# Performance work log

Hardware: AMD Instinct MI355X
Metric: run time of the kernel (lower is better)

Reference implementation:

```python
import jax, jax.numpy as jnp
import numpy as np

B, D, O = 512, 256, 128  # batch, input_dim, output_dim


def setup_inputs() -> dict:
    key = jax.random.key(0)
    k1, k2, k3, k4, k5, k6 = jax.random.split(key, 6)
    eyeD = jnp.eye(D, dtype=jnp.float32)
    # density-like inputs: diagonal offset keeps the trace denominator well-conditioned
    x_real = jax.random.normal(k1, (B, D, D), dtype=jnp.float32) + 2.0 * eyeD
    x_imag = jax.random.normal(k2, (B, D, D), dtype=jnp.float32)
    # weight = identity + small perturbation (module inits to [eye, zeros] stacked)
    w_r = eyeD + 0.02 * jax.random.normal(k3, (D, D), dtype=jnp.float32)
    w_i = 0.02 * jax.random.normal(k4, (D, D), dtype=jnp.float32)
    weight = jnp.stack([w_r, w_i], axis=-1)  # [D, D, 2]
    rand_w = jax.random.uniform(k5, (O,), dtype=jnp.float32)
    lam = jax.random.uniform(k6, (1,), dtype=jnp.float32)
    return {"x_real": x_real, "x_imag": x_imag, "weight": weight,
            "rand_w": rand_w, "lam": lam}


def reference(x_real, x_imag, weight, rand_w, lam):
    out_dim = rand_w.shape[0]
    U_r = weight[:, :, 0]  # [D, D]
    U_i = weight[:, :, 1]
    # evolution: (U_r + i U_i) X (U_r + i U_i)^H, batched over b
    R = jnp.einsum('ij,bjk->bik', U_r, x_real) - jnp.einsum('ij,bjk->bik', U_i, x_imag)
    I = jnp.einsum('ij,bjk->bik', U_i, x_real) + jnp.einsum('ij,bjk->bik', U_r, x_imag)
    out_r = jnp.einsum('bik,jk->bij', R, U_r) + jnp.einsum('bik,jk->bij', I, U_i)
    out_i = jnp.einsum('bik,jk->bij', I, U_r) - jnp.einsum('bik,jk->bij', R, U_i)
    # input_dim >= output_dim branch: top-left block, normalized by trace of real part
    sub_r = out_r[:, :out_dim, :out_dim]
    sub_i = out_i[:, :out_dim, :out_dim]
    tr = jnp.trace(sub_r, axis1=1, axis2=2)[:, None, None]  # [B,1,1]
    norm_r = sub_r / tr
    norm_i = sub_i / tr
    p = jax.nn.softmax(rand_w, axis=-1)
    s = jax.nn.sigmoid(lam[0])
    output_r = s * norm_r + (1.0 - s) * jnp.diag(p)
    output_i = s * norm_i
    return (output_r, output_i)
```

## Files before the change

### kernel.cpp

```cpp
#include <hip/hip_runtime.h>
#include <hip/hip_bf16.h>


typedef __attribute__((ext_vector_type(4))) float f32x4;
typedef __attribute__((ext_vector_type(8))) short bf16x8;

static __device__ __forceinline__ short f2bf(float f) {
    unsigned u = __float_as_uint(f);
    u += 0x7fffu + ((u >> 16) & 1u);
    return (short)(u >> 16);
}

static __device__ __forceinline__ unsigned cvtpk2(float lo, float hi) {
    union { __hip_bfloat162 h; unsigned u; } c;
    c.h = __float22bfloat162_rn(float2{lo, hi});
    return c.u;
}

static __device__ __forceinline__ bf16x8 pack8(f32x4 a, f32x4 b) {
    union { unsigned u[4]; bf16x8 v; } r;
    r.u[0] = cvtpk2(a[0], a[1]);
    r.u[1] = cvtpk2(a[2], a[3]);
    r.u[2] = cvtpk2(b[0], b[1]);
    r.u[3] = cvtpk2(b[2], b[3]);
    return r.v;
}

static __device__ __forceinline__ f32x4 mfma16(bf16x8 a, bf16x8 b, f32x4 c) {
    return __builtin_amdgcn_mfma_f32_16x16x32_bf16(a, b, c, 0, 0, 0);
}

#define XGOFF(S) (((S) >> 3) * 16384 + ((S) & 7) * 32)

__global__ void qprep_u(const float* __restrict__ wt,
                        short* __restrict__ Ur, short* __restrict__ Ui) {
    int idx = blockIdx.x * 256 + threadIdx.x;
    float2 v = ((const float2*)wt)[idx];
    Ur[idx] = f2bf(v.x);
    Ui[idx] = f2bf(v.y);
}

__global__ void qprep_ps(const float* __restrict__ rw, const float* __restrict__ lm,
                         float* __restrict__ pv, float* __restrict__ sv) {
    int t = threadIdx.x;
    float w0 = rw[t], w1 = rw[t + 64];
    float m = fmaxf(w0, w1);
    #pragma unroll
    for (int o = 32; o > 0; o >>= 1) m = fmaxf(m, __shfl_xor(m, o));
    float e0 = expf(w0 - m), e1 = expf(w1 - m);
    float ss = e0 + e1;
    #pragma unroll
    for (int o = 32; o > 0; o >>= 1) ss += __shfl_xor(ss, o);
    pv[t] = e0 / ss;
    pv[t + 64] = e1 / ss;
    if (t == 0) sv[0] = 1.f / (1.f + expf(-lm[0]));
}

__global__ void qprep_q(const float* __restrict__ wt,
                        short* __restrict__ Qrb, short* __restrict__ Qib) {
    int j = blockIdx.x;
    int k = threadIdx.x;
    float ar = 0.f, ai = 0.f;
    for (int i = 0; i < 128; ++i) {
        float2 uk = ((const float2*)wt)[i * 256 + k];
        float2 uj = ((const float2*)wt)[i * 256 + j];
        ar += uk.x * uj.x + uk.y * uj.y;
        ai += uk.x * uj.y - uk.y * uj.x;
    }
    Qrb[j * 256 + k] = f2bf(ar);
    Qib[j * 256 + k] = f2bf(ai);
}

template<int P>
static __device__ __forceinline__ void phaseT(
    char* smem, const float* xgR, const float* xgI, int stW,
    int rdo0, int rdo1, const short* qbr, const short* qbi,
    int kb, int c16, int g4, bool dotr,
    f32x4* genR, f32x4* genI, bf16x8* qgr, bf16x8* qgi,
    f32x4* yR, f32x4* yI, f32x4& tr4)
{
    if (P + 1 < 32) {
        char* sb = smem + 65536 + ((P + 1) & 1) * 16384;
        *(f32x4*)(sb + stW)        = genR[(P + 1) & 3];
        *(f32x4*)(sb + 8192 + stW) = genI[(P + 1) & 3];
    }
    if (dotr && (P + 1 < 32)) {
        qgr[(P + 1) & 1] = *(const bf16x8*)(qbr + XGOFF(P + 1));
        qgi[(P + 1) & 1] = *(const bf16x8*)(qbi + XGOFF(P + 1));
    }
    if (P + 5 < 32) {
        genR[(P + 5) & 3] = *(const f32x4*)(xgR + XGOFF(P + 5));
        genI[(P + 5) & 3] = *(const f32x4*)(xgI + XGOFF(P + 5));
    }
    asm volatile("" ::: "memory");
    {
        char* rb = smem + 65536 + (P & 1) * 16384;
        f32x4 a0 = *(const f32x4*)(rb + rdo0);
        f32x4 a1 = *(const f32x4*)(rb + rdo1);
        f32x4 b0 = *(const f32x4*)(rb + 8192 + rdo0);
        f32x4 b1 = *(const f32x4*)(rb + 8192 + rdo1);
        bf16x8 axr  = pack8(a0, a1);
        bf16x8 axi  = pack8(b0, b1);
        bf16x8 axrn = axr ^ (short)0x8000;
        {
            const int kloc = kb + c16;
            const int uo = kloc * 512 + (((P & 7) * 64 + g4 * 16) ^ ((kloc & 7) << 4));
            bf16x8 bur = *(const bf16x8*)(smem + uo);
            bf16x8 bui = *(const bf16x8*)(smem + 32768 + uo);
            yR[0] = mfma16(axr,  bur, yR[0]);
            yR[0] = mfma16(axi,  bui, yR[0]);
            yI[0] = mfma16(axi,  bur, yI[0]);
            yI[0] = mfma16(axrn, bui, yI[0]);
        }
        {
            const int kloc = kb + 16 + c16;
            const int uo = kloc * 512 + (((P & 7) * 64 + g4 * 16) ^ ((kloc & 7) << 4));
            bf16x8 bur = *(const bf16x8*)(smem + uo);
            bf16x8 bui = *(const bf16x8*)(smem + 32768 + uo);
            yR[1] = mfma16(axr,  bur, yR[1]);
            yR[1] = mfma16(axi,  bui, yR[1]);
            yI[1] = mfma16(axi,  bur, yI[1]);
            yI[1] = mfma16(axrn, bui, yI[1]);
        }
        if (dotr) {
            bf16x8 axin = axi ^ (short)0x8000;
            tr4 = mfma16(axr,  qgr[P & 1], tr4);
            tr4 = mfma16(axin, qgi[P & 1], tr4);
        }
    }
    asm volatile("s_waitcnt lgkmcnt(0)" ::: "memory");
    __builtin_amdgcn_sched_barrier(0);
    __builtin_amdgcn_s_barrier();
    __builtin_amdgcn_sched_barrier(0);
}

static __device__ __forceinline__ void stageB(
    char* smem, const short* Urg, const short* Uig, int jt,
    int wm, int wn, int c16, int g4,
    f32x4 (&sR)[2][2], f32x4 (&sI)[2][2])
{
    #pragma unroll
    for (int ks2 = 0; ks2 < 2; ++ks2) {
        bf16x8 aur[2], aui[2], auin[2];
        #pragma unroll
        for (int mt = 0; mt < 2; ++mt) {
            int i = wm * 32 + mt * 16 + c16;
            aur[mt]  = *(const bf16x8*)(Urg + (size_t)i * 256 + jt + ks2 * 32 + g4 * 8);
            aui[mt]  = *(const bf16x8*)(Uig + (size_t)i * 256 + jt + ks2 * 32 + g4 * 8);
            auin[mt] = aui[mt] ^ (short)0x8000;
        }
        #pragma unroll
        for (int nt2 = 0; nt2 < 2; ++nt2) {
            int kloc = wn * 32 + nt2 * 16 + c16;
            int off  = kloc * 128 + ((ks2 * 64 + g4 * 16) ^ ((kloc & 7) << 4));
            bf16x8 byr = *(const bf16x8*)(smem + 98304 + off);
            bf16x8 byi = *(const bf16x8*)(smem + 106496 + off);
            #pragma unroll
            for (int mt = 0; mt < 2; ++mt) {
                sR[mt][nt2] = mfma16(aur[mt],  byr, sR[mt][nt2]);
                sR[mt][nt2] = mfma16(auin[mt], byi, sR[mt][nt2]);
                sI[mt][nt2] = mfma16(aui[mt],  byr, sI[mt][nt2]);
                sI[mt][nt2] = mfma16(aur[mt],  byi, sI[mt][nt2]);
            }
        }
    }
}

#define YT_AND_B(JT) do {                                                       \
    {                                                                           \
        const int klA = kb + c16;                                               \
        const int oA  = klA * 128 + ((ja * 2 + g4 * 8) ^ ((klA & 7) << 4));     \
        uint2 v;                                                                \
        v.x = cvtpk2(yR[0][0], yR[0][1]); v.y = cvtpk2(yR[0][2], yR[0][3]);     \
        *(uint2*)(smem + 98304 + oA) = v;                                       \
        v.x = cvtpk2(yI[0][0], yI[0][1]); v.y = cvtpk2(yI[0][2], yI[0][3]);     \
        *(uint2*)(smem + 106496 + oA) = v;                                      \
        const int klB = kb + 16 + c16;                                          \
        const int oB  = klB * 128 + ((ja * 2 + g4 * 8) ^ ((klB & 7) << 4));     \
        v.x = cvtpk2(yR[1][0], yR[1][1]); v.y = cvtpk2(yR[1][2], yR[1][3]);     \
        *(uint2*)(smem + 98304 + oB) = v;                                       \
        v.x = cvtpk2(yI[1][0], yI[1][1]); v.y = cvtpk2(yI[1][2], yI[1][3]);     \
        *(uint2*)(smem + 106496 + oB) = v;                                      \
    }                                                                           \
    asm volatile("s_waitcnt lgkmcnt(0)" ::: "memory");                          \
    __builtin_amdgcn_sched_barrier(0);                                          \
    __builtin_amdgcn_s_barrier();                                               \
    __builtin_amdgcn_sched_barrier(0);                                          \
    stageB(smem, Urg, Uig, (JT) * 64, wm, wn, c16, g4, sR, sI);                 \
    yR[0] = zero; yR[1] = zero; yI[0] = zero; yI[1] = zero;                     \
} while (0)

#define PH(P) phaseT<P>(smem, xgR, xgI, stW, rdo0, rdo1, qbr, qbi, kb, c16, g4, \
                        dotr, genR, genI, qgr, qgi, yR, yI, tr4)

__global__ __launch_bounds__(512, 2) void qfused(
    const float* __restrict__ xr, const float* __restrict__ xi,
    const short* __restrict__ Urg, const short* __restrict__ Uig,
    const short* __restrict__ Qrb, const short* __restrict__ Qib,
    const float* __restrict__ pv, const float* __restrict__ sv,
    float* __restrict__ out)
{
    __shared__ __align__(16) char smem[114688];

    const int bx   = blockIdx.x;
    const int b    = bx >> 1;
    const int kh   = bx & 1;
    const int tid  = threadIdx.x;
    const int lane = tid & 63;
    const int w    = tid >> 6;
    const int c16  = lane & 15;
    const int g4   = lane >> 4;

    #pragma unroll
    for (int q = 0; q < 4; ++q) {
        int c    = tid + q * 512;
        int row  = c >> 5;
        int slot = c & 31;
        int ss   = slot ^ (row & 7);
        const short* sr = Urg + (size_t)(kh * 64 + row) * 256 + ss * 8;
        const short* si = Uig + (size_t)(kh * 64 + row) * 256 + ss * 8;
        *(bf16x8*)(smem + row * 512 + slot * 16)         = *(const bf16x8*)sr;
        *(bf16x8*)(smem + 32768 + row * 512 + slot * 16) = *(const bf16x8*)si;
    }

    const float* xrb = xr + ((size_t)b << 16);
    const float* xib = xi + ((size_t)b << 16);

    const int  ja   = (w & 3) * 16;
    const int  kb   = (w >> 2) * 32;
    const int  wm   = w >> 1;
    const int  wn   = w & 1;
    const bool dotr = (w < 4);

    const int rowW = w * 8 + (lane >> 3);
    const int cW   = lane & 7;
    const float* xgR = xrb + rowW * 256 + cW * 4;
    const float* xgI = xib + rowW * 256 + cW * 4;
    const int stW  = rowW * 128 + ((cW ^ (rowW & 7)) << 4);

    const int rA   = ja + c16;
    const int rdo0 = rA * 128 + (((2 * g4)     ^ (rA & 7)) << 4);
    const int rdo1 = rA * 128 + (((2 * g4 + 1) ^ (rA & 7)) << 4);

    const short* qbr = Qrb + (size_t)(ja + c16) * 256 + g4 * 8;
    const short* qbi = Qib + (size_t)(ja + c16) * 256 + g4 * 8;

    f32x4 zero = {0.f, 0.f, 0.f, 0.f};
    f32x4 sR[2][2], sI[2][2];
    #pragma unroll
    for (int m = 0; m < 2; ++m)
        #pragma unroll
        for (int n = 0; n < 2; ++n) { sR[m][n] = zero; sI[m][n] = zero; }
    f32x4 tr4 = zero;
    f32x4 yR[2], yI[2];
    yR[0] = zero; yR[1] = zero; yI[0] = zero; yI[1] = zero;

    f32x4 genR[4], genI[4];
    bf16x8 qgr[2], qgi[2];

    {
        f32x4 t0R = *(const f32x4*)(xgR + XGOFF(0));
        f32x4 t0I = *(const f32x4*)(xgI + XGOFF(0));
        genR[1] = *(const f32x4*)(xgR + XGOFF(1));
        genI[1] = *(const f32x4*)(xgI + XGOFF(1));
        genR[2] = *(const f32x4*)(xgR + XGOFF(2));
        genI[2] = *(const f32x4*)(xgI + XGOFF(2));
        genR[3] = *(const f32x4*)(xgR + XGOFF(3));
        genI[3] = *(const f32x4*)(xgI + XGOFF(3));
        genR[0] = *(const f32x4*)(xgR + XGOFF(4));
        genI[0] = *(const f32x4*)(xgI + XGOFF(4));
        if (dotr) {
            qgr[0] = *(const bf16x8*)(qbr + XGOFF(0));
            qgi[0] = *(const bf16x8*)(qbi + XGOFF(0));
        }
        *(f32x4*)(smem + 65536 + stW)        = t0R;
        *(f32x4*)(smem + 65536 + 8192 + stW) = t0I;
    }
    __syncthreads();

    PH(0);  PH(1);  PH(2);  PH(3);  PH(4);  PH(5);  PH(6);  PH(7);
    YT_AND_B(0);
    PH(8);  PH(9);  PH(10); PH(11); PH(12); PH(13); PH(14); PH(15);
    YT_AND_B(1);
    PH(16); PH(17); PH(18); PH(19); PH(20); PH(21); PH(22); PH(23);
    YT_AND_B(2);
    PH(24); PH(25); PH(26); PH(27); PH(28); PH(29); PH(30); PH(31);
    YT_AND_B(3);

    float loc = (dotr && ((c16 >> 2) == g4)) ? tr4[c16 & 3] : 0.f;
    #pragma unroll
    for (int o = 32; o > 0; o >>= 1) loc += __shfl_xor(loc, o);
    __syncthreads();
    float* red = (float*)(smem + 65536);
    if (lane == 0) red[w] = loc;
    __syncthreads();
    float tr = red[0] + red[1] + red[2] + red[3] + red[4] + red[5] + red[6] + red[7];

    float s     = sv[0];
    float inv   = s / tr;
    float onems = 1.f - s;
    float* outr = out + (size_t)b * 16384;
    float* outi = out + 8388608 + (size_t)b * 16384;

    #pragma unroll
    for (int mt = 0; mt < 2; ++mt)
        #pragma unroll
        for (int nt2 = 0; nt2 < 2; ++nt2) {
            int colc = kh * 64 + wn * 32 + nt2 * 16 + c16;
            #pragma unroll
            for (int r = 0; r < 4; ++r) {
                int row = wm * 32 + mt * 16 + g4 * 4 + r;
                float vr = sR[mt][nt2][r] * inv;
                if (row == colc) vr += onems * pv[row];
                outr[row * 128 + colc] = vr;
                outi[row * 128 + colc] = sI[mt][nt2][r] * inv;
            }
        }
}

extern "C" void kernel_launch(void* const* d_in, const int* in_sizes, int n_in,
                              void* d_out, int out_size, void* d_ws, size_t ws_size,
                              hipStream_t stream) {
    (void)in_sizes; (void)n_in; (void)out_size; (void)ws_size;
    const float* xr = (const float*)d_in[0];
    const float* xi = (const float*)d_in[1];
    const float* wt = (const float*)d_in[2];
    const float* rw = (const float*)d_in[3];
    const float* lm = (const float*)d_in[4];

    short* Ur  = (short*)d_ws;
    short* Ui  = Ur + 32768;
    float* pv  = (float*)((char*)d_ws + 131072);
    float* sv  = pv + 128;
    short* Qrb = (short*)((char*)d_ws + 135168);
    short* Qib = (short*)((char*)d_ws + 266240);
    float* o   = (float*)d_out;

    qprep_u<<<dim3(128), dim3(256), 0, stream>>>(wt, Ur, Ui);
    qprep_ps<<<dim3(1), dim3(64), 0, stream>>>(rw, lm, pv, sv);
    qprep_q<<<dim3(256), dim3(256), 0, stream>>>(wt, Qrb, Qib);
    qfused<<<dim3(1024), dim3(512), 0, stream>>>(xr, xi, Ur, Ui, Qrb, Qib, pv, sv, o);
}
```

Baseline: 175.4 us.

## Load X fragments directly from global into MFMA layout, drop LDS staging

```diff
diff --git a/kernel.cpp b/kernel.cpp
--- a/kernel.cpp
+++ b/kernel.cpp
@@ -73,69 +73,57 @@
 
 template<int P>
 static __device__ __forceinline__ void phaseT(
-    char* smem, const float* xgR, const float* xgI, int stW,
-    int rdo0, int rdo1, const short* qbr, const short* qbi,
+    const char* smem, const float* xgR, const float* xgI,
+    const short* qbr, const short* qbi,
     int kb, int c16, int g4, bool dotr,
-    f32x4* genR, f32x4* genI, bf16x8* qgr, bf16x8* qgi,
+    f32x4* gRa, f32x4* gRb, f32x4* gIa, f32x4* gIb,
+    bf16x8* qgr, bf16x8* qgi,
     f32x4* yR, f32x4* yI, f32x4& tr4)
 {
-    if (P + 1 < 32) {
-        char* sb = smem + 65536 + ((P + 1) & 1) * 16384;
-        *(f32x4*)(sb + stW)        = genR[(P + 1) & 3];
-        *(f32x4*)(sb + 8192 + stW) = genI[(P + 1) & 3];
+    if (P + 2 < 32) {
+        constexpr int S = (P + 2 < 32) ? P + 2 : 0;
+        gRa[S % 3] = *(const f32x4*)(xgR + XGOFF(S));
+        gRb[S % 3] = *(const f32x4*)(xgR + XGOFF(S) + 4);
+        gIa[S % 3] = *(const f32x4*)(xgI + XGOFF(S));
+        gIb[S % 3] = *(const f32x4*)(xgI + XGOFF(S) + 4);
     }
     if (dotr && (P + 1 < 32)) {
         qgr[(P + 1) & 1] = *(const bf16x8*)(qbr + XGOFF(P + 1));
         qgi[(P + 1) & 1] = *(const bf16x8*)(qbi + XGOFF(P + 1));
     }
-    if (P + 5 < 32) {
-        genR[(P + 5) & 3] = *(const f32x4*)(xgR + XGOFF(P + 5));
-        genI[(P + 5) & 3] = *(const f32x4*)(xgI + XGOFF(P + 5));
-    }
     asm volatile("" ::: "memory");
+    bf16x8 axr  = pack8(gRa[P % 3], gRb[P % 3]);
+    bf16x8 axi  = pack8(gIa[P % 3], gIb[P % 3]);
+    bf16x8 axrn = axr ^ (short)0x8000;
     {
-        char* rb = smem + 65536 + (P & 1) * 16384;
-        f32x4 a0 = *(const f32x4*)(rb + rdo0);
-        f32x4 a1 = *(const f32x4*)(rb + rdo1);
-        f32x4 b0 = *(const f32x4*)(rb + 8192 + rdo0);
-        f32x4 b1 = *(const f32x4*)(rb + 8192 + rdo1);
-        bf16x8 axr  = pack8(a0, a1);
-        bf16x8 axi  = pack8(b0, b1);
-        bf16x8 axrn = axr ^ (short)0x8000;
-        {
-            const int kloc = kb + c16;
-            const int uo = kloc * 512 + (((P & 7) * 64 + g4 * 16) ^ ((kloc & 7) << 4));
-            bf16x8 bur = *(const bf16x8*)(smem + uo);
-            bf16x8 bui = *(const bf16x8*)(smem + 32768 + uo);
-            yR[0] = mfma16(axr,  bur, yR[0]);
-            yR[0] = mfma16(axi,  bui, yR[0]);
-            yI[0] = mfma16(axi,  bur, yI[0]);
-            yI[0] = mfma16(axrn, bui, yI[0]);
-        }
-        {
-            const int kloc = kb + 16 + c16;
-            const int uo = kloc * 512 + (((P & 7) * 64 + g4 * 16) ^ ((kloc & 7) << 4));
-            bf16x8 bur = *(const bf16x8*)(smem + uo);
-            bf16x8 bui = *(const bf16x8*)(smem + 32768 + uo);
-            yR[1] = mfma16(axr,  bur, yR[1]);
-            yR[1] = mfma16(axi,  bui, yR[1]);
-            yI[1] = mfma16(axi,  bur, yI[1]);
-            yI[1] = mfma16(axrn, bui, yI[1]);
-        }
-        if (dotr) {
-            bf16x8 axin = axi ^ (short)0x8000;
-            tr4 = mfma16(axr,  qgr[P & 1], tr4);
-            tr4 = mfma16(axin, qgi[P & 1], tr4);
-        }
-    }
-    asm volatile("s_waitcnt lgkmcnt(0)" ::: "memory");
-    __builtin_amdgcn_sched_barrier(0);
-    __builtin_amdgcn_s_barrier();
-    __builtin_amdgcn_sched_barrier(0);
+        const int kloc = kb + c16;
+        const int uo = kloc * 512 + (((P & 7) * 64 + g4 * 16) ^ ((kloc & 7) << 4));
+        bf16x8 bur = *(const bf16x8*)(smem + uo);
+        bf16x8 bui = *(const bf16x8*)(smem + 32768 + uo);
+        yR[0] = mfma16(axr,  bur, yR[0]);
+        yR[0] = mfma16(axi,  bui, yR[0]);
+        yI[0] = mfma16(axi,  bur, yI[0]);
+        yI[0] = mfma16(axrn, bui, yI[0]);
+    }
+    {
+        const int kloc = kb + 16 + c16;
+        const int uo = kloc * 512 + (((P & 7) * 64 + g4 * 16) ^ ((kloc & 7) << 4));
+        bf16x8 bur = *(const bf16x8*)(smem + uo);
+        bf16x8 bui = *(const bf16x8*)(smem + 32768 + uo);
+        yR[1] = mfma16(axr,  bur, yR[1]);
+        yR[1] = mfma16(axi,  bui, yR[1]);
+        yI[1] = mfma16(axi,  bur, yI[1]);
+        yI[1] = mfma16(axrn, bui, yI[1]);
+    }
+    if (dotr) {
+        bf16x8 axin = axi ^ (short)0x8000;
+        tr4 = mfma16(axr,  qgr[P & 1], tr4);
+        tr4 = mfma16(axin, qgi[P & 1], tr4);
+    }
 }
 
 static __device__ __forceinline__ void stageB(
-    char* smem, const short* Urg, const short* Uig, int jt,
+    const char* smem, const short* Urg, const short* Uig, int jt,
     int wm, int wn, int c16, int g4,
     f32x4 (&sR)[2][2], f32x4 (&sI)[2][2])
 {
@@ -153,8 +141,8 @@
         for (int nt2 = 0; nt2 < 2; ++nt2) {
             int kloc = wn * 32 + nt2 * 16 + c16;
             int off  = kloc * 128 + ((ks2 * 64 + g4 * 16) ^ ((kloc & 7) << 4));
-            bf16x8 byr = *(const bf16x8*)(smem + 98304 + off);
-            bf16x8 byi = *(const bf16x8*)(smem + 106496 + off);
+            bf16x8 byr = *(const bf16x8*)(smem + 65536 + off);
+            bf16x8 byi = *(const bf16x8*)(smem + 73728 + off);
             #pragma unroll
             for (int mt = 0; mt < 2; ++mt) {
                 sR[mt][nt2] = mfma16(aur[mt],  byr, sR[mt][nt2]);
@@ -167,20 +155,22 @@
 }
 
 #define YT_AND_B(JT) do {                                                       \
+    __builtin_amdgcn_s_barrier();                                               \
+    __builtin_amdgcn_sched_barrier(0);                                          \
     {                                                                           \
         const int klA = kb + c16;                                               \
         const int oA  = klA * 128 + ((ja * 2 + g4 * 8) ^ ((klA & 7) << 4));     \
         uint2 v;                                                                \
         v.x = cvtpk2(yR[0][0], yR[0][1]); v.y = cvtpk2(yR[0][2], yR[0][3]);     \
-        *(uint2*)(smem + 98304 + oA) = v;                                       \
+        *(uint2*)(smem + 65536 + oA) = v;                                       \
         v.x = cvtpk2(yI[0][0], yI[0][1]); v.y = cvtpk2(yI[0][2], yI[0][3]);     \
-        *(uint2*)(smem + 106496 + oA) = v;                                      \
+        *(uint2*)(smem + 73728 + oA) = v;                                       \
         const int klB = kb + 16 + c16;                                          \
         const int oB  = klB * 128 + ((ja * 2 + g4 * 8) ^ ((klB & 7) << 4));     \
         v.x = cvtpk2(yR[1][0], yR[1][1]); v.y = cvtpk2(yR[1][2], yR[1][3]);     \
-        *(uint2*)(smem + 98304 + oB) = v;                                       \
+        *(uint2*)(smem + 65536 + oB) = v;                                       \
         v.x = cvtpk2(yI[1][0], yI[1][1]); v.y = cvtpk2(yI[1][2], yI[1][3]);     \
-        *(uint2*)(smem + 106496 + oB) = v;                                      \
+        *(uint2*)(smem + 73728 + oB) = v;                                       \
     }                                                                           \
     asm volatile("s_waitcnt lgkmcnt(0)" ::: "memory");                          \
     __builtin_amdgcn_sched_barrier(0);                                          \
@@ -190,17 +180,17 @@
     yR[0] = zero; yR[1] = zero; yI[0] = zero; yI[1] = zero;                     \
 } while (0)
 
-#define PH(P) phaseT<P>(smem, xgR, xgI, stW, rdo0, rdo1, qbr, qbi, kb, c16, g4, \
-                        dotr, genR, genI, qgr, qgi, yR, yI, tr4)
-
-__global__ __launch_bounds__(512, 2) void qfused(
+#define PH(P) phaseT<P>(smem, xgR, xgI, qbr, qbi, kb, c16, g4, dotr,            \
+                        gRa, gRb, gIa, gIb, qgr, qgi, yR, yI, tr4)
+
+__global__ __launch_bounds__(512, 4) void qfused(
     const float* __restrict__ xr, const float* __restrict__ xi,
     const short* __restrict__ Urg, const short* __restrict__ Uig,
     const short* __restrict__ Qrb, const short* __restrict__ Qib,
     const float* __restrict__ pv, const float* __restrict__ sv,
     float* __restrict__ out)
 {
-    __shared__ __align__(16) char smem[114688];
+    __shared__ __align__(16) char smem[81920];
 
     const int bx   = blockIdx.x;
     const int b    = bx >> 1;
@@ -232,16 +222,8 @@
     const int  wn   = w & 1;
     const bool dotr = (w < 4);
 
-    const int rowW = w * 8 + (lane >> 3);
-    const int cW   = lane & 7;
-    const float* xgR = xrb + rowW * 256 + cW * 4;
-    const float* xgI = xib + rowW * 256 + cW * 4;
-    const int stW  = rowW * 128 + ((cW ^ (rowW & 7)) << 4);
-
-    const int rA   = ja + c16;
-    const int rdo0 = rA * 128 + (((2 * g4)     ^ (rA & 7)) << 4);
-    const int rdo1 = rA * 128 + (((2 * g4 + 1) ^ (rA & 7)) << 4);
-
+    const float* xgR = xrb + (size_t)(ja + c16) * 256 + g4 * 8;
+    const float* xgI = xib + (size_t)(ja + c16) * 256 + g4 * 8;
     const short* qbr = Qrb + (size_t)(ja + c16) * 256 + g4 * 8;
     const short* qbi = Qib + (size_t)(ja + c16) * 256 + g4 * 8;
 
@@ -255,28 +237,25 @@
     f32x4 yR[2], yI[2];
     yR[0] = zero; yR[1] = zero; yI[0] = zero; yI[1] = zero;
 
-    f32x4 genR[4], genI[4];
+    f32x4 gRa[3], gRb[3], gIa[3], gIb[3];
     bf16x8 qgr[2], qgi[2];
 
-    {
-        f32x4 t0R = *(const f32x4*)(xgR + XGOFF(0));
-        f32x4 t0I = *(const f32x4*)(xgI + XGOFF(0));
-        genR[1] = *(const f32x4*)(xgR + XGOFF(1));
-        genI[1] = *(const f32x4*)(xgI + XGOFF(1));
-        genR[2] = *(const f32x4*)(xgR + XGOFF(2));
-        genI[2] = *(const f32x4*)(xgI + XGOFF(2));
-        genR[3] = *(const f32x4*)(xgR + XGOFF(3));
-        genI[3] = *(const f32x4*)(xgI + XGOFF(3));
-        genR[0] = *(const f32x4*)(xgR + XGOFF(4));
-        genI[0] = *(const f32x4*)(xgI + XGOFF(4));
-        if (dotr) {
-            qgr[0] = *(const bf16x8*)(qbr + XGOFF(0));
-            qgi[0] = *(const bf16x8*)(qbi + XGOFF(0));
-        }
-        *(f32x4*)(smem + 65536 + stW)        = t0R;
-        *(f32x4*)(smem + 65536 + 8192 + stW) = t0I;
-    }
-    __syncthreads();
+    gRa[0] = *(const f32x4*)(xgR + XGOFF(0));
+    gRb[0] = *(const f32x4*)(xgR + XGOFF(0) + 4);
+    gIa[0] = *(const f32x4*)(xgI + XGOFF(0));
+    gIb[0] = *(const f32x4*)(xgI + XGOFF(0) + 4);
+    gRa[1] = *(const f32x4*)(xgR + XGOFF(1));
+    gRb[1] = *(const f32x4*)(xgR + XGOFF(1) + 4);
+    gIa[1] = *(const f32x4*)(xgI + XGOFF(1));
+    gIb[1] = *(const f32x4*)(xgI + XGOFF(1) + 4);
+    if (dotr) {
+        qgr[0] = *(const bf16x8*)(qbr + XGOFF(0));
+        qgi[0] = *(const bf16x8*)(qbi + XGOFF(0));
+    }
+    asm volatile("s_waitcnt lgkmcnt(0)" ::: "memory");
+    __builtin_amdgcn_sched_barrier(0);
+    __builtin_amdgcn_s_barrier();
+    __builtin_amdgcn_sched_barrier(0);
 
     PH(0);  PH(1);  PH(2);  PH(3);  PH(4);  PH(5);  PH(6);  PH(7);
     YT_AND_B(0);
```

Result: slower. 313.8 us (+78.9%).
